# Kernel optimization log

Hardware: AMD Instinct MI355X
Metric: run time of the kernel (lower is better)

Reference implementation:

```python
import jax, jax.numpy as jnp
import numpy as np

NEG_INF = -1e30  # stand-in for float('-inf') that is safe under softmax


def setup_inputs() -> dict:
    key = jax.random.key(0)
    k1, k2, k3, k4 = jax.random.split(key, 4)
    B, T, C, H = 4, 4096, 1024, 128
    x = jax.random.normal(k1, (B, T, C), dtype=jnp.float32)
    # nn.Linear(n_emb, head_size, bias=False): store as [C, H] so y = x @ W
    Wk = jax.random.normal(k2, (C, H), dtype=jnp.float32) * (C ** -0.5)
    Wq = jax.random.normal(k3, (C, H), dtype=jnp.float32) * (C ** -0.5)
    Wv = jax.random.normal(k4, (C, H), dtype=jnp.float32) * (C ** -0.5)
    return {"x": x, "Wk": Wk, "Wq": Wq, "Wv": Wv}


def reference(x, Wk, Wq, Wv):
    B, T, C = x.shape
    k = x @ Wk  # [B, T, H]
    q = x @ Wq  # [B, T, H]
    v = x @ Wv  # [B, T, H]
    # Faithful to original: wei = k @ q^T, scaled by C**-0.5 (C = n_emb)
    wei = jnp.einsum('bih,bjh->bij', k, q) * (C ** -0.5)  # [B, T, T]
    causal = jnp.tril(jnp.ones((T, T), dtype=bool))
    wei = jnp.where(causal, wei, NEG_INF)
    wei = jax.nn.softmax(wei, axis=-1)
    out = jnp.einsum('bij,bjh->bih', wei, v)  # [B, T, H]
    return out
```

## Files before the change

kernel.cpp:

```cpp
#include <hip/hip_runtime.h>
#include <hip/hip_bf16.h>

#define T_SEQ 4096
#define NBATCH 4
#define C_EMB 1024
#define H_DIM 128
#define M_ROWS (NBATCH * T_SEQ)
#define SPLIT 4

typedef __bf16 bf16x8 __attribute__((ext_vector_type(8)));
typedef float  floatx4 __attribute__((ext_vector_type(4)));

__device__ __forceinline__ ushort f2bf(float f) {
    __hip_bfloat16 h = __float2bfloat16(f);
    return *reinterpret_cast<ushort*>(&h);
}
__device__ __forceinline__ float bf2f(ushort u) {
    unsigned int v = ((unsigned int)u) << 16;
    return *reinterpret_cast<float*>(&v);
}
__device__ __forceinline__ uint4 pack8(const float4& a, const float4& b) {
    __hip_bfloat162 h0 = __float22bfloat162_rn(make_float2(a.x, a.y));
    __hip_bfloat162 h1 = __float22bfloat162_rn(make_float2(a.z, a.w));
    __hip_bfloat162 h2 = __float22bfloat162_rn(make_float2(b.x, b.y));
    __hip_bfloat162 h3 = __float22bfloat162_rn(make_float2(b.z, b.w));
    uint4 r;
    r.x = *reinterpret_cast<unsigned int*>(&h0);
    r.y = *reinterpret_cast<unsigned int*>(&h1);
    r.z = *reinterpret_cast<unsigned int*>(&h2);
    r.w = *reinterpret_cast<unsigned int*>(&h3);
    return r;
}
__device__ __forceinline__ void gld16(const ushort* g, ushort* l) {
    __builtin_amdgcn_global_load_lds(
        (const __attribute__((address_space(1))) unsigned int*)(g),
        (__attribute__((address_space(3))) unsigned int*)(l),
        16, 0, 0);
}

__global__ __launch_bounds__(256) void transpose_w(
    const float* __restrict__ Wk, const float* __restrict__ Wq,
    const float* __restrict__ Wv, ushort* __restrict__ wt) {
    const int z = blockIdx.z;
    const float* W = (z == 0) ? Wk : (z == 1) ? Wq : Wv;
    const int k0 = blockIdx.x * 64;
    const int n0 = blockIdx.y * 64;

    __shared__ ushort tile[64][72];

    const int tid = threadIdx.x;
    const int c4 = tid & 15;
    const int rg = tid >> 4;
#pragma unroll
    for (int i = 0; i < 4; ++i) {
        int r = rg * 4 + i;
        float4 v = *reinterpret_cast<const float4*>(
            W + (size_t)(k0 + r) * H_DIM + n0 + c4 * 4);
        tile[r][c4 * 4 + 0] = f2bf(v.x);
        tile[r][c4 * 4 + 1] = f2bf(v.y);
        tile[r][c4 * 4 + 2] = f2bf(v.z);
        tile[r][c4 * 4 + 3] = f2bf(v.w);
    }
    __syncthreads();
    ushort* Wtz = wt + (size_t)z * H_DIM * C_EMB;
#pragma unroll
    for (int o = 0; o < 2; ++o) {
        int linear = o * 256 + tid;
        int nl = linear >> 3;
        int kc = linear & 7;
        ushort e[8];
#pragma unroll
        for (int j = 0; j < 8; ++j) e[j] = tile[kc * 8 + j][nl];
        uint4 pk;
        pk.x = (unsigned int)e[0] | ((unsigned int)e[1] << 16);
        pk.y = (unsigned int)e[2] | ((unsigned int)e[3] << 16);
        pk.z = (unsigned int)e[4] | ((unsigned int)e[5] << 16);
        pk.w = (unsigned int)e[6] | ((unsigned int)e[7] << 16);
        *reinterpret_cast<uint4*>(
            Wtz + (size_t)(n0 + nl) * C_EMB + k0 + kc * 8) = pk;
    }
}

__global__ __launch_bounds__(512, 1) void qkv_gemm(
    const float* __restrict__ x, const ushort* __restrict__ wt,
    ushort* __restrict__ kqv) {
    const int m0 = blockIdx.x * 64;

    __shared__ ushort As[2][64 * 64];
    __shared__ ushort Bs[2][384 * 64];

    const int tid  = threadIdx.x;
    const int lane = tid & 63;
    const int wave = tid >> 6;
    const int l15  = lane & 15;
    const int quad = lane >> 4;
    const int mg   = (wave >> 1) * 16;
    const int nb   = (wave & 1) * 12;

    floatx4 acc[12];
#pragma unroll
    for (int nj = 0; nj < 12; ++nj) acc[nj] = floatx4{0.f, 0.f, 0.f, 0.f};

    const int ar = tid >> 3;
    const int ac = tid & 7;
    const int chp = ac ^ (ar & 7);
    const float* xrow = x + (size_t)(m0 + ar) * C_EMB + ac * 8;

    float4 xa = *reinterpret_cast<const float4*>(xrow);
    float4 xb = *reinterpret_cast<const float4*>(xrow + 4);
#pragma unroll
    for (int i = 0; i < 6; ++i) {
        int rbase = wave * 48 + i * 8;
        int row = rbase + (lane >> 3);
        int chg = (lane & 7) ^ (row & 7);
        gld16(wt + (size_t)row * C_EMB + chg * 8, Bs[0] + rbase * 64);
    }
    *reinterpret_cast<uint4*>(As[0] + ar * 64 + chp * 8) = pack8(xa, xb);
    __syncthreads();
    xa = *reinterpret_cast<const float4*>(xrow + 64);
    xb = *reinterpret_cast<const float4*>(xrow + 68);

    for (int kt = 0; kt < 16; ++kt) {
        const int cur = kt & 1;

        if (kt < 15) {
#pragma unroll
            for (int i = 0; i < 6; ++i) {
                int rbase = wave * 48 + i * 8;
                int row = rbase + (lane >> 3);
                int chg = (lane & 7) ^ (row & 7);
                gld16(wt + (size_t)row * C_EMB + (kt + 1) * 64 + chg * 8,
                      Bs[cur ^ 1] + rbase * 64);
            }
            *reinterpret_cast<uint4*>(As[cur ^ 1] + ar * 64 + chp * 8) = pack8(xa, xb);
        }
        if (kt < 14) {
            const float* nsrc = xrow + (kt + 2) * 64;
            xa = *reinterpret_cast<const float4*>(nsrc);
            xb = *reinterpret_cast<const float4*>(nsrc + 4);
        }

#pragma unroll
        for (int kk = 0; kk < 2; ++kk) {
            bf16x8 a = *reinterpret_cast<const bf16x8*>(
                As[cur] + (mg + l15) * 64 + ((4 * kk + quad) ^ (l15 & 7)) * 8);
#pragma unroll
            for (int nj = 0; nj < 12; ++nj) {
                int brow = (nb + nj) * 16 + l15;
                bf16x8 b = *reinterpret_cast<const bf16x8*>(
                    Bs[cur] + brow * 64 + ((4 * kk + quad) ^ (brow & 7)) * 8);
                acc[nj] = __builtin_amdgcn_mfma_f32_16x16x32_bf16(a, b, acc[nj], 0, 0, 0);
            }
        }

        __syncthreads();
    }

    const int rowb = m0 + mg + quad * 4;
#pragma unroll
    for (int nj = 0; nj < 12; ++nj) {
        int gcol = (nb + nj) * 16 + l15;
        int z = gcol >> 7;
        int cz = gcol & 127;
        if (z < 2) {
            const float scale = (z == 0) ? 0.03125f : 1.0f;
            ushort* outz = kqv + (size_t)z * M_ROWS * H_DIM;
#pragma unroll
            for (int r = 0; r < 4; ++r)
                outz[(size_t)(rowb + r) * H_DIM + cz] = f2bf(acc[nj][r] * scale);
        } else {
            ushort* vt = kqv + (size_t)2 * M_ROWS * H_DIM;
            int bb   = rowb >> 12;
            int tloc = rowb & (T_SEQ - 1);
            ushort4 pk;
            pk.x = f2bf(acc[nj][0]);
            pk.y = f2bf(acc[nj][1]);
            pk.z = f2bf(acc[nj][2]);
            pk.w = f2bf(acc[nj][3]);
            *reinterpret_cast<ushort4*>(
                vt + ((size_t)(bb * H_DIM + cz) << 12) + tloc) = pk;
        }
    }
}

#define P_STRIDE 72
__global__ __launch_bounds__(256, 3) void flash_chunk(
    const ushort* __restrict__ kqv, ushort* __restrict__ partO,
    float* __restrict__ partML) {
    const int it = 63 - (blockIdx.x >> 2);
    const int c  = blockIdx.x & 3;
    if (c > it) return;
    const int b  = blockIdx.y;
    const int i0 = it * 64;

    const ushort* Qg = kqv + (size_t)b * T_SEQ * H_DIM;
    const ushort* Kg = kqv + (size_t)M_ROWS * H_DIM + (size_t)b * T_SEQ * H_DIM;
    const ushort* Vt = kqv + (size_t)2 * M_ROWS * H_DIM + (size_t)b * H_DIM * T_SEQ;

    __shared__ ushort Ks[64 * 128];
    __shared__ ushort Vs[128 * 64];
    __shared__ ushort Ps[4][16 * P_STRIDE];

    const int tid  = threadIdx.x;
    const int lane = tid & 63;
    const int wave = tid >> 6;
    const int l15  = lane & 15;
    const int quad = lane >> 4;

    bf16x8 q[4];
    {
        const ushort* qrow = Qg + (size_t)(i0 + wave * 16 + l15) * H_DIM + quad * 8;
#pragma unroll
        for (int kk = 0; kk < 4; ++kk)
            q[kk] = *reinterpret_cast<const bf16x8*>(qrow + kk * 32);
    }

    float m_i[4], l_i[4];
#pragma unroll
    for (int r = 0; r < 4; ++r) { m_i[r] = -1e30f; l_i[r] = 0.f; }
    floatx4 o[8];
#pragma unroll
    for (int nh = 0; nh < 8; ++nh) o[nh] = floatx4{0.f, 0.f, 0.f, 0.f};

    ushort* Pw = Ps[wave];

    for (int jt = c; jt <= it; jt += SPLIT) {
        const int j0 = jt * 64;
        __syncthreads();
#pragma unroll
        for (int i = 0; i < 4; ++i) {
            int row = wave * 16 + i * 4 + (lane >> 4);
            int chg = (lane & 15) ^ (row & 15);
            gld16(Kg + (size_t)(j0 + row) * H_DIM + chg * 8,
                  Ks + (wave * 16 + i * 4) * 128);
        }
#pragma unroll
        for (int i = 0; i < 4; ++i) {
            int row = wave * 32 + i * 8 + (lane >> 3);
            int chg = (lane & 7) ^ (row & 7);
            gld16(Vt + (size_t)row * T_SEQ + j0 + chg * 8,
                  Vs + (wave * 32 + i * 8) * 64);
        }
        __syncthreads();

        floatx4 s[4];
#pragma unroll
        for (int ni = 0; ni < 4; ++ni) s[ni] = floatx4{0.f, 0.f, 0.f, 0.f};
        __builtin_amdgcn_s_setprio(1);
#pragma unroll
        for (int kk = 0; kk < 4; ++kk)
#pragma unroll
            for (int ni = 0; ni < 4; ++ni) {
                bf16x8 kb = *reinterpret_cast<const bf16x8*>(
                    Ks + (ni * 16 + l15) * 128 + ((4 * kk + quad) ^ l15) * 8);
                s[ni] = __builtin_amdgcn_mfma_f32_16x16x32_bf16(q[kk], kb, s[ni], 0, 0, 0);
            }
        __builtin_amdgcn_s_setprio(0);

        if (jt == it) {
            int ii = i0 + wave * 16 + quad * 4;
#pragma unroll
            for (int ni = 0; ni < 4; ++ni) {
                int j = j0 + ni * 16 + l15;
#pragma unroll
                for (int r = 0; r < 4; ++r)
                    if (j > ii + r) s[ni][r] = -1e30f;
            }
        }

        float alpha[4], rs[4];
#pragma unroll
        for (int r = 0; r < 4; ++r) {
            float v = fmaxf(fmaxf(s[0][r], s[1][r]), fmaxf(s[2][r], s[3][r]));
#pragma unroll
            for (int off = 8; off >= 1; off >>= 1)
                v = fmaxf(v, __shfl_xor(v, off, 64));
            float mn = fmaxf(m_i[r], v);
            alpha[r] = __expf(m_i[r] - mn);
            m_i[r] = mn;
            rs[r] = 0.f;
        }
#pragma unroll
        for (int ni = 0; ni < 4; ++ni)
#pragma unroll
            for (int r = 0; r < 4; ++r) {
                float p = __expf(s[ni][r] - m_i[r]);
                rs[r] += p;
                Pw[(quad * 4 + r) * P_STRIDE + ni * 16 + l15] = f2bf(p);
            }
#pragma unroll
        for (int r = 0; r < 4; ++r) {
            float v = rs[r];
#pragma unroll
            for (int off = 8; off >= 1; off >>= 1)
                v += __shfl_xor(v, off, 64);
            l_i[r] = l_i[r] * alpha[r] + v;
        }
#pragma unroll
        for (int nh = 0; nh < 8; ++nh)
#pragma unroll
            for (int r = 0; r < 4; ++r) o[nh][r] *= alpha[r];

#pragma unroll
        for (int kp = 0; kp < 2; ++kp) {
            bf16x8 a = *reinterpret_cast<const bf16x8*>(
                Pw + l15 * P_STRIDE + kp * 32 + quad * 8);
            __builtin_amdgcn_s_setprio(1);
#pragma unroll
            for (int nh = 0; nh < 8; ++nh) {
                bf16x8 vb = *reinterpret_cast<const bf16x8*>(
                    Vs + (nh * 16 + l15) * 64 + ((4 * kp + quad) ^ (l15 & 7)) * 8);
                o[nh] = __builtin_amdgcn_mfma_f32_16x16x32_bf16(a, vb, o[nh], 0, 0, 0);
            }
            __builtin_amdgcn_s_setprio(0);
        }
    }

    const int idx = ((b * 64 + it) << 2) + c;
    ushort* po = partO + (size_t)idx * 64 * 128;
#pragma unroll
    for (int nh = 0; nh < 8; ++nh)
#pragma unroll
        for (int r = 0; r < 4; ++r) {
            int row = wave * 16 + quad * 4 + r;
            po[(size_t)row * 128 + nh * 16 + l15] = f2bf(o[nh][r]);
        }
    if (l15 == 0) {
        float* ml = partML + (size_t)idx * 128;
#pragma unroll
        for (int r = 0; r < 4; ++r) {
            int row = wave * 16 + quad * 4 + r;
            ml[row]      = m_i[r];
            ml[64 + row] = l_i[r];
        }
    }
}

__global__ __launch_bounds__(256) void combine(
    const ushort* __restrict__ partO, const float* __restrict__ partML,
    float* __restrict__ out) {
    const int it = blockIdx.x >> 2;
    const int qr = blockIdx.x & 3;
    const int b  = blockIdx.y;
    const int count = min(SPLIT, it + 1);
    const int tid = threadIdx.x;
    const int row = qr * 16 + (tid >> 4);
    const int cg  = (tid & 15) * 8;
    const int base = (b * 64 + it) << 2;

    float m_c[SPLIT], l_c[SPLIT];
    float M = -1e30f;
    for (int cc = 0; cc < count; ++cc) {
        const float* ml = partML + (size_t)(base + cc) * 128;
        m_c[cc] = ml[row];
        l_c[cc] = ml[64 + row];
        M = fmaxf(M, m_c[cc]);
    }
    float L = 0.f, w[SPLIT];
    for (int cc = 0; cc < count; ++cc) {
        w[cc] = __expf(m_c[cc] - M);
        L += w[cc] * l_c[cc];
    }

    float acc[8];
#pragma unroll
    for (int j = 0; j < 8; ++j) acc[j] = 0.f;
    for (int cc = 0; cc < count; ++cc) {
        const ushort* po = partO + (size_t)(base + cc) * 8192 + (size_t)row * 128 + cg;
        uint4 v = *reinterpret_cast<const uint4*>(po);
        const ushort* pv = reinterpret_cast<const ushort*>(&v);
        float wc = w[cc];
#pragma unroll
        for (int e = 0; e < 8; ++e)
            acc[e] += wc * bf2f(pv[e]);
    }
    float invL = 1.0f / L;
    float* op = out + ((size_t)b * T_SEQ + it * 64 + row) * H_DIM + cg;
    float4 v0, v1;
    v0.x = acc[0] * invL; v0.y = acc[1] * invL;
    v0.z = acc[2] * invL; v0.w = acc[3] * invL;
    v1.x = acc[4] * invL; v1.y = acc[5] * invL;
    v1.z = acc[6] * invL; v1.w = acc[7] * invL;
    *reinterpret_cast<float4*>(op)     = v0;
    *reinterpret_cast<float4*>(op + 4) = v1;
}

extern "C" void kernel_launch(void* const* d_in, const int* in_sizes, int n_in,
                              void* d_out, int out_size, void* d_ws, size_t ws_size,
                              hipStream_t stream) {
    const float* x  = (const float*)d_in[0];
    const float* Wk = (const float*)d_in[1];
    const float* Wq = (const float*)d_in[2];
    const float* Wv = (const float*)d_in[3];

    ushort* kqv    = (ushort*)d_ws;
    ushort* wt     = kqv + (size_t)3 * M_ROWS * H_DIM;
    ushort* partO  = wt + (size_t)3 * H_DIM * C_EMB;
    float*  partML = (float*)(partO + (size_t)1024 * 64 * 128);

    transpose_w<<<dim3(16, 2, 3), 256, 0, stream>>>(Wk, Wq, Wv, wt);
    qkv_gemm<<<dim3(256), 512, 0, stream>>>(x, wt, kqv);
    flash_chunk<<<dim3(64 * SPLIT, NBATCH), 256, 0, stream>>>(kqv, partO, partML);
    combine<<<dim3(256, NBATCH), 256, 0, stream>>>(partO, partML, (float*)d_out);
}
```

Measured before the change: 178.2 us.

## Double-buffer K tiles in LDS and load V straight into registers

The K tile now lives in two LDS buffers. The next chunk's K is prefetched with async global-to-LDS loads while the current chunk is computed, which removes the second barrier per iteration. V is no longer staged in LDS: each wave reads its V fragments directly from global memory into registers before the QK^T MFMAs. This hides load latency and cuts LDS traffic, but each wave now reads the full V tile redundantly through cache and holds 64 extra VGPRs, which could hurt occupancy under the 3-blocks launch bound.

```diff
diff --git a/kernel.cpp b/kernel.cpp
--- a/kernel.cpp
+++ b/kernel.cpp
@@ -197,8 +197,7 @@
     const ushort* Kg = kqv + (size_t)M_ROWS * H_DIM + (size_t)b * T_SEQ * H_DIM;
     const ushort* Vt = kqv + (size_t)2 * M_ROWS * H_DIM + (size_t)b * H_DIM * T_SEQ;
 
-    __shared__ ushort Ks[64 * 128];
-    __shared__ ushort Vs[128 * 64];
+    __shared__ ushort Ks[2][64 * 128];
     __shared__ ushort Ps[4][16 * P_STRIDE];
 
     const int tid  = threadIdx.x;
@@ -223,25 +222,45 @@
     for (int nh = 0; nh < 8; ++nh) o[nh] = floatx4{0.f, 0.f, 0.f, 0.f};
 
     ushort* Pw = Ps[wave];
+    const ushort* Vbase = Vt + (size_t)l15 * T_SEQ + quad * 8;
+
+    const int krow = lane >> 4;
+    const int kchg = (lane & 15);
+
+    {
+        const int j0s = c * 64;
+#pragma unroll
+        for (int i = 0; i < 4; ++i) {
+            int row = wave * 16 + i * 4 + krow;
+            int chg = kchg ^ (row & 15);
+            gld16(Kg + (size_t)(j0s + row) * H_DIM + chg * 8,
+                  Ks[0] + (wave * 16 + i * 4) * 128);
+        }
+    }
+    int cur = 0;
 
     for (int jt = c; jt <= it; jt += SPLIT) {
         const int j0 = jt * 64;
         __syncthreads();
-#pragma unroll
-        for (int i = 0; i < 4; ++i) {
-            int row = wave * 16 + i * 4 + (lane >> 4);
-            int chg = (lane & 15) ^ (row & 15);
-            gld16(Kg + (size_t)(j0 + row) * H_DIM + chg * 8,
-                  Ks + (wave * 16 + i * 4) * 128);
-        }
-#pragma unroll
-        for (int i = 0; i < 4; ++i) {
-            int row = wave * 32 + i * 8 + (lane >> 3);
-            int chg = (lane & 7) ^ (row & 7);
-            gld16(Vt + (size_t)row * T_SEQ + j0 + chg * 8,
-                  Vs + (wave * 32 + i * 8) * 64);
-        }
-        __syncthreads();
+
+        if (jt + SPLIT <= it) {
+            const int j0n = (jt + SPLIT) * 64;
+#pragma unroll
+            for (int i = 0; i < 4; ++i) {
+                int row = wave * 16 + i * 4 + krow;
+                int chg = kchg ^ (row & 15);
+                gld16(Kg + (size_t)(j0n + row) * H_DIM + chg * 8,
+                      Ks[cur ^ 1] + (wave * 16 + i * 4) * 128);
+            }
+        }
+
+        bf16x8 vb[2][8];
+#pragma unroll
+        for (int kp = 0; kp < 2; ++kp)
+#pragma unroll
+            for (int nh = 0; nh < 8; ++nh)
+                vb[kp][nh] = *reinterpret_cast<const bf16x8*>(
+                    Vbase + (size_t)(nh * 16) * T_SEQ + j0 + kp * 32);
 
         floatx4 s[4];
 #pragma unroll
@@ -252,7 +271,7 @@
 #pragma unroll
             for (int ni = 0; ni < 4; ++ni) {
                 bf16x8 kb = *reinterpret_cast<const bf16x8*>(
-                    Ks + (ni * 16 + l15) * 128 + ((4 * kk + quad) ^ l15) * 8);
+                    Ks[cur] + (ni * 16 + l15) * 128 + ((4 * kk + quad) ^ l15) * 8);
                 s[ni] = __builtin_amdgcn_mfma_f32_16x16x32_bf16(q[kk], kb, s[ni], 0, 0, 0);
             }
         __builtin_amdgcn_s_setprio(0);
@@ -307,13 +326,12 @@
                 Pw + l15 * P_STRIDE + kp * 32 + quad * 8);
             __builtin_amdgcn_s_setprio(1);
 #pragma unroll
-            for (int nh = 0; nh < 8; ++nh) {
-                bf16x8 vb = *reinterpret_cast<const bf16x8*>(
-                    Vs + (nh * 16 + l15) * 64 + ((4 * kp + quad) ^ (l15 & 7)) * 8);
-                o[nh] = __builtin_amdgcn_mfma_f32_16x16x32_bf16(a, vb, o[nh], 0, 0, 0);
-            }
+            for (int nh = 0; nh < 8; ++nh)
+                o[nh] = __builtin_amdgcn_mfma_f32_16x16x32_bf16(a, vb[kp][nh], o[nh], 0, 0, 0);
             __builtin_amdgcn_s_setprio(0);
         }
+
+        cur ^= 1;
     }
 
     const int idx = ((b * 64 + it) << 2) + c;
```

Result: slower. 235.3 us (+32.0%).

## Split causal KV range into fixed-size contiguous chunks per query tile

Applied to the files above, without the earlier changes.

Replaces the 4-way strided KV split with contiguous chunks of at most 11 KV tiles, so long query rows get more chunks and short rows fewer. A triangular slot indexing packs the partial outputs, and combine merges a variable number of partials (up to 6). This is meant to cap per-block work and even out the causal load imbalance. In exchange it launches more blocks and adds more partial-output traffic for the combine step.

```diff
diff --git a/kernel.cpp b/kernel.cpp
--- a/kernel.cpp
+++ b/kernel.cpp
@@ -6,7 +6,9 @@
 #define C_EMB 1024
 #define H_DIM 128
 #define M_ROWS (NBATCH * T_SEQ)
-#define SPLIT 4
+#define CH 11
+#define MAXCH 6
+#define SLOTS_PER_B 219
 
 typedef __bf16 bf16x8 __attribute__((ext_vector_type(8)));
 typedef float  floatx4 __attribute__((ext_vector_type(4)));
@@ -36,6 +38,10 @@
         (const __attribute__((address_space(1))) unsigned int*)(g),
         (__attribute__((address_space(3))) unsigned int*)(l),
         16, 0, 0);
+}
+__device__ __forceinline__ int slot_base(int it) {
+    int q = it / CH, r = it % CH;
+    return CH * q * (q + 1) / 2 + r * (q + 1);
 }
 
 __global__ __launch_bounds__(256) void transpose_w(
@@ -187,9 +193,12 @@
 __global__ __launch_bounds__(256, 3) void flash_chunk(
     const ushort* __restrict__ kqv, ushort* __restrict__ partO,
     float* __restrict__ partML) {
-    const int it = 63 - (blockIdx.x >> 2);
-    const int c  = blockIdx.x & 3;
-    if (c > it) return;
+    const int bx = blockIdx.x;
+    const int it = 63 - (bx / MAXCH);
+    const int c  = bx % MAXCH;
+    const int jlo = c * CH;
+    if (jlo > it) return;
+    const int jhi = min(jlo + CH, it + 1);
     const int b  = blockIdx.y;
     const int i0 = it * 64;
 
@@ -224,7 +233,7 @@
 
     ushort* Pw = Ps[wave];
 
-    for (int jt = c; jt <= it; jt += SPLIT) {
+    for (int jt = jlo; jt < jhi; ++jt) {
         const int j0 = jt * 64;
         __syncthreads();
 #pragma unroll
@@ -316,7 +325,7 @@
         }
     }
 
-    const int idx = ((b * 64 + it) << 2) + c;
+    const int idx = b * SLOTS_PER_B + slot_base(it) + c;
     ushort* po = partO + (size_t)idx * 64 * 128;
 #pragma unroll
     for (int nh = 0; nh < 8; ++nh)
@@ -342,13 +351,13 @@
     const int it = blockIdx.x >> 2;
     const int qr = blockIdx.x & 3;
     const int b  = blockIdx.y;
-    const int count = min(SPLIT, it + 1);
+    const int count = (it + CH) / CH;
     const int tid = threadIdx.x;
     const int row = qr * 16 + (tid >> 4);
     const int cg  = (tid & 15) * 8;
-    const int base = (b * 64 + it) << 2;
-
-    float m_c[SPLIT], l_c[SPLIT];
+    const int base = b * SLOTS_PER_B + slot_base(it);
+
+    float m_c[MAXCH], l_c[MAXCH];
     float M = -1e30f;
     for (int cc = 0; cc < count; ++cc) {
         const float* ml = partML + (size_t)(base + cc) * 128;
@@ -356,7 +365,7 @@
         l_c[cc] = ml[64 + row];
         M = fmaxf(M, m_c[cc]);
     }
-    float L = 0.f, w[SPLIT];
+    float L = 0.f, w[MAXCH];
     for (int cc = 0; cc < count; ++cc) {
         w[cc] = __expf(m_c[cc] - M);
         L += w[cc] * l_c[cc];
@@ -396,10 +405,10 @@
     ushort* kqv    = (ushort*)d_ws;
     ushort* wt     = kqv + (size_t)3 * M_ROWS * H_DIM;
     ushort* partO  = wt + (size_t)3 * H_DIM * C_EMB;
-    float*  partML = (float*)(partO + (size_t)1024 * 64 * 128);
+    float*  partML = (float*)(partO + (size_t)(NBATCH * SLOTS_PER_B) * 64 * 128);
 
     transpose_w<<<dim3(16, 2, 3), 256, 0, stream>>>(Wk, Wq, Wv, wt);
     qkv_gemm<<<dim3(256), 512, 0, stream>>>(x, wt, kqv);
-    flash_chunk<<<dim3(64 * SPLIT, NBATCH), 256, 0, stream>>>(kqv, partO, partML);
+    flash_chunk<<<dim3(64 * MAXCH, NBATCH), 256, 0, stream>>>(kqv, partO, partML);
     combine<<<dim3(256, NBATCH), 256, 0, stream>>>(partO, partML, (float*)d_out);
 }
```

Result: slower. 185.6 us (+4.1%).
